# Optimization experiments

Hardware: AMD Instinct MI355X
Metric: run time of the kernel (lower is better)

Reference implementation:

```python
import jax, jax.numpy as jnp
import numpy as np

N, E = 50000, 800000
IN_DIM, OUT_DIM, REL_DIM = 128, 64, 32
NEG_SLOPE = 0.01  # torch F.leaky_relu default


def setup_inputs() -> dict:
    key = jax.random.key(0)
    ks = jax.random.split(key, 12)
    return {
        "h": jax.random.normal(ks[0], (N, IN_DIM), jnp.float32),
        "relation": jax.random.normal(ks[1], (E, REL_DIM), jnp.float32),
        "score": jax.random.normal(ks[2], (E, 1), jnp.float32),
        "timestamp": jax.random.normal(ks[3], (E, 1), jnp.float32),
        "src": jax.random.randint(ks[4], (E,), 0, N, jnp.int32),
        "dst": jax.random.randint(ks[5], (E,), 0, N, jnp.int32),
        "W_n": jax.random.normal(ks[6], (IN_DIM, OUT_DIM), jnp.float32) / np.sqrt(IN_DIM),
        "W_r": jax.random.normal(ks[7], (REL_DIM, OUT_DIM), jnp.float32) / np.sqrt(REL_DIM),
        "W_s": jax.random.normal(ks[8], (1, OUT_DIM), jnp.float32),
        "W_t": jax.random.normal(ks[9], (1, OUT_DIM), jnp.float32),
        "a": jax.random.normal(ks[10], (5 * OUT_DIM,), jnp.float32) / np.sqrt(5 * OUT_DIM),
    }


def reference(h, relation, score, timestamp, src, dst, W_n, W_r, W_s, W_t, a):
    D = W_n.shape[1]
    z = h @ W_n                     # (N, D)
    er = relation @ W_r             # (E, D)
    es = score @ W_s                # (E, D)
    et = timestamp @ W_t            # (E, D)
    z_src = z[src]                  # (E, D) gather
    z_dst = z[dst]                  # (E, D) gather
    # attn_fc on concat([z_src, z_dst, er, es, et]) == sum of slice dot-products
    a1, a2, a3, a4, a5 = (a[0:D], a[D:2*D], a[2*D:3*D], a[3*D:4*D], a[4*D:5*D])
    logit = z_src @ a1 + z_dst @ a2 + er @ a3 + es @ a4 + et @ a5  # (E,)
    logit = jnp.where(logit >= 0, logit, NEG_SLOPE * logit)        # leaky_relu
    # segment softmax over edges grouped by dst node
    n = z.shape[0]
    seg_max = jax.ops.segment_max(logit, dst, num_segments=n)     # (N,)
    ex = jnp.exp(logit - seg_max[dst])                             # (E,)
    seg_sum = jax.ops.segment_sum(ex, dst, num_segments=n)        # (N,)
    alpha = ex / seg_sum[dst]                                      # (E,)
    # weighted scatter-sum of source features to dst nodes
    h_out = jax.ops.segment_sum(alpha[:, None] * z_src, dst, num_segments=n)  # (N, D)
    return h_out
```

## Files before the change

### kernel.cpp

```cpp
#include <hip/hip_runtime.h>

#define IN_DIM 128
#define OUT_DIM 64
#define REL_DIM 32
#define NEG_SLOPE 0.01f

__global__ void k_consts(const float* __restrict__ W_r, const float* __restrict__ W_s,
                         const float* __restrict__ W_t, const float* __restrict__ a,
                         float* __restrict__ consts ) {
    int t = threadIdx.x;
    if (t < REL_DIM) {
        const float* a3 = a + 2 * OUT_DIM;
        float acc = 0.f;
        for (int d = 0; d < OUT_DIM; ++d) acc += W_r[t * OUT_DIM + d] * a3[d];
        consts[t] = acc;
    } else if (t == 32) {
        float acc = 0.f;
        for (int d = 0; d < OUT_DIM; ++d) acc += W_s[d] * a[3 * OUT_DIM + d];
        consts[32] = acc;
    } else if (t == 33) {
        float acc = 0.f;
        for (int d = 0; d < OUT_DIM; ++d) acc += W_t[d] * a[4 * OUT_DIM + d];
        consts[33] = acc;
    }
}

__global__ __launch_bounds__(256) void k_node(const float* __restrict__ h,
                                              const float* __restrict__ W_n,
                                              const float* __restrict__ a,
                                              float* __restrict__ z,
                                              float* __restrict__ s1,
                                              float* __restrict__ s2, int n) {
    __shared__ float hs[IN_DIM * 65];
    __shared__ float s1p[4][64], s2p[4][64];
    int base = blockIdx.x * 64;

    for (int i = threadIdx.x; i < 64 * 32; i += 256) {
        int r = i >> 5;
        int c4 = i & 31;
        float4 v = make_float4(0.f, 0.f, 0.f, 0.f);
        if (base + r < n) v = ((const float4*)(h + (size_t)(base + r) * IN_DIM))[c4];
        int k0 = c4 * 4;
        hs[(k0 + 0) * 65 + r] = v.x;
        hs[(k0 + 1) * 65 + r] = v.y;
        hs[(k0 + 2) * 65 + r] = v.z;
        hs[(k0 + 3) * 65 + r] = v.w;
    }
    __syncthreads();

    int lane = threadIdx.x & 63;
    int w = __builtin_amdgcn_readfirstlane(threadIdx.x >> 6);
    int c0 = w * 16;
    int row = base + lane;

    float acc[16];
    #pragma unroll
    for (int j = 0; j < 16; ++j) acc[j] = 0.f;

    const float* __restrict__ Wslice = W_n + c0;
    #pragma unroll 4
    for (int k = 0; k < IN_DIM; ++k) {
        float hv = hs[k * 65 + lane];
        const float* __restrict__ Wr = Wslice + k * OUT_DIM;
        #pragma unroll
        for (int j = 0; j < 16; ++j) acc[j] = fmaf(hv, Wr[j], acc[j]);
    }

    float p1 = 0.f, p2 = 0.f;
    #pragma unroll
    for (int j = 0; j < 16; ++j) {
        p1 = fmaf(acc[j], a[c0 + j], p1);
        p2 = fmaf(acc[j], a[OUT_DIM + c0 + j], p2);
    }
    s1p[w][lane] = p1;
    s2p[w][lane] = p2;

    if (row < n) {
        float4* zp = (float4*)(z + (size_t)row * OUT_DIM + c0);
        zp[0] = make_float4(acc[0], acc[1], acc[2], acc[3]);
        zp[1] = make_float4(acc[4], acc[5], acc[6], acc[7]);
        zp[2] = make_float4(acc[8], acc[9], acc[10], acc[11]);
        zp[3] = make_float4(acc[12], acc[13], acc[14], acc[15]);
    }
    __syncthreads();
    if (threadIdx.x < 64 && base + (int)threadIdx.x < n) {
        int l = threadIdx.x;
        s1[base + l] = s1p[0][l] + s1p[1][l] + s1p[2][l] + s1p[3][l];
        s2[base + l] = s2p[0][l] + s2p[1][l] + s2p[2][l] + s2p[3][l];
    }
}

__global__ __launch_bounds__(256) void k_count(const int* __restrict__ dst,
                                               int* __restrict__ deg, int E) {
    for (int e = blockIdx.x * blockDim.x + threadIdx.x; e < E;
         e += gridDim.x * blockDim.x)
        atomicAdd(deg + dst[e], 1);
}

__global__ __launch_bounds__(256) void k_scan1(const int* __restrict__ deg,
                                               int* __restrict__ incl,
                                               int* __restrict__ partial, int n) {
    __shared__ int tmp[256];
    int i = blockIdx.x * 256 + threadIdx.x;
    int v = (i < n) ? deg[i] : 0;
    tmp[threadIdx.x] = v;
    __syncthreads();
    #pragma unroll
    for (int o = 1; o < 256; o <<= 1) {
        int t = (threadIdx.x >= o) ? tmp[threadIdx.x - o] : 0;
        __syncthreads();
        tmp[threadIdx.x] += t;
        __syncthreads();
    }
    if (i < n) incl[i] = tmp[threadIdx.x];
    if (threadIdx.x == 255) partial[blockIdx.x] = tmp[255];
}

__global__ __launch_bounds__(256) void k_scan2(int* __restrict__ partial, int nb) {
    __shared__ int tmp[256];
    int v = (threadIdx.x < nb) ? partial[threadIdx.x] : 0;
    tmp[threadIdx.x] = v;
    __syncthreads();
    #pragma unroll
    for (int o = 1; o < 256; o <<= 1) {
        int t = (threadIdx.x >= o) ? tmp[threadIdx.x - o] : 0;
        __syncthreads();
        tmp[threadIdx.x] += t;
        __syncthreads();
    }
    if (threadIdx.x < nb) partial[threadIdx.x] = tmp[threadIdx.x] - v;
}

__global__ __launch_bounds__(256) void k_scan3(const int* __restrict__ deg,
                                               const int* __restrict__ incl,
                                               const int* __restrict__ partial,
                                               int* __restrict__ off,
                                               int* __restrict__ cnt, int n, int E) {
    int i = blockIdx.x * 256 + threadIdx.x;
    if (i < n) {
        int o = incl[i] - deg[i] + partial[i >> 8];
        off[i] = o;
        cnt[i] = o;
    }
    if (i == 0) off[n] = E;
}

__global__ __launch_bounds__(256) void k_fill(const float* __restrict__ rel,
                                              const float* __restrict__ score,
                                              const float* __restrict__ ts,
                                              const int* __restrict__ src,
                                              const int* __restrict__ dst,
                                              const float* __restrict__ s1,
                                              const float* __restrict__ s2,
                                              const float* __restrict__ consts,
                                              int* __restrict__ cnt,
                                              int2* __restrict__ pedge, int E) {
    __shared__ float wra3[REL_DIM];
    __shared__ float c45[2];
    if (threadIdx.x < REL_DIM) wra3[threadIdx.x] = consts[threadIdx.x];
    if (threadIdx.x == 32) c45[0] = consts[32];
    if (threadIdx.x == 33) c45[1] = consts[33];
    __syncthreads();
    for (int e = blockIdx.x * blockDim.x + threadIdx.x; e < E;
         e += gridDim.x * blockDim.x) {
        const float4* r4 = (const float4*)(rel + (size_t)e * REL_DIM);
        float acc = 0.f;
        #pragma unroll
        for (int j = 0; j < REL_DIM / 4; ++j) {
            float4 v = r4[j];
            acc += v.x * wra3[4 * j] + v.y * wra3[4 * j + 1] +
                   v.z * wra3[4 * j + 2] + v.w * wra3[4 * j + 3];
        }
        int s = src[e], d = dst[e];
        float lg = s1[s] + s2[d] + acc + score[e] * c45[0] + ts[e] * c45[1];
        lg = (lg >= 0.f) ? lg : NEG_SLOPE * lg;
        int pos = atomicAdd(cnt + d, 1);
        pedge[pos] = make_int2(s, __float_as_int(lg));
    }
}

__global__ __launch_bounds__(256) void k_out(const int* __restrict__ off,
                                             const int2* __restrict__ pedge,
                                             const float* __restrict__ z,
                                             float* __restrict__ out, int n) {
    int lane = threadIdx.x & 63;
    int wave = (blockIdx.x * blockDim.x + threadIdx.x) >> 6;
    int nwaves = (gridDim.x * blockDim.x) >> 6;
    int eg = lane >> 4;
    int dl = lane & 15;
    for (int node = wave; node < n; node += nwaves) {
        int start = off[node], end = off[node + 1];
        int deg = end - start;
        float4 acc = make_float4(0.f, 0.f, 0.f, 0.f);
        if (deg > 0 && deg <= 64) {
            int2 pe = make_int2(0, (int)0xff800000u);
            if (lane < deg) pe = pedge[start + lane];
            float v = __int_as_float(pe.y);
            float m = v;
            #pragma unroll
            for (int o = 32; o > 0; o >>= 1) m = fmaxf(m, __shfl_xor(m, o, 64));
            float ex = __expf(v - m);
            float ssum = ex;
            #pragma unroll
            for (int o = 32; o > 0; o >>= 1) ssum += __shfl_xor(ssum, o, 64);
            float alpha = ex * (1.0f / ssum);
            for (int j0 = 0; j0 < deg; j0 += 4) {
                int j = j0 + eg;
                int jc = (j < 64) ? j : 63;
                float wj = __shfl(alpha, jc, 64);
                int  sj = __shfl(pe.x, jc, 64);
                if (j < deg) {
                    float4 zv = ((const float4*)(z + (size_t)sj * OUT_DIM))[dl];
                    acc.x = fmaf(wj, zv.x, acc.x);
                    acc.y = fmaf(wj, zv.y, acc.y);
                    acc.z = fmaf(wj, zv.z, acc.z);
                    acc.w = fmaf(wj, zv.w, acc.w);
                }
            }
        } else if (deg > 64) {
            float m = -3.4e38f;
            for (int j = start + lane; j < end; j += 64)
                m = fmaxf(m, __int_as_float(pedge[j].y));
            #pragma unroll
            for (int o = 32; o > 0; o >>= 1) m = fmaxf(m, __shfl_xor(m, o, 64));
            float ssum = 0.f;
            for (int j = start + lane; j < end; j += 64)
                ssum += __expf(__int_as_float(pedge[j].y) - m);
            #pragma unroll
            for (int o = 32; o > 0; o >>= 1) ssum += __shfl_xor(ssum, o, 64);
            float inv = 1.0f / ssum;
            for (int j0 = start; j0 < end; j0 += 4) {
                int j = j0 + eg;
                if (j < end) {
                    int2 pe = pedge[j];
                    float wj = __expf(__int_as_float(pe.y) - m) * inv;
                    float4 zv = ((const float4*)(z + (size_t)pe.x * OUT_DIM))[dl];
                    acc.x = fmaf(wj, zv.x, acc.x);
                    acc.y = fmaf(wj, zv.y, acc.y);
                    acc.z = fmaf(wj, zv.z, acc.z);
                    acc.w = fmaf(wj, zv.w, acc.w);
                }
            }
        }
        #pragma unroll
        for (int o = 16; o <= 32; o <<= 1) {
            acc.x += __shfl_xor(acc.x, o, 64);
            acc.y += __shfl_xor(acc.y, o, 64);
            acc.z += __shfl_xor(acc.z, o, 64);
            acc.w += __shfl_xor(acc.w, o, 64);
        }
        if (eg == 0) ((float4*)(out + (size_t)node * OUT_DIM))[dl] = acc;
    }
}

extern "C" void kernel_launch(void* const* d_in, const int* in_sizes, int n_in,
                              void* d_out, int out_size, void* d_ws, size_t ws_size,
                              hipStream_t stream) {
    const float* h         = (const float*)d_in[0];
    const float* relation  = (const float*)d_in[1];
    const float* score     = (const float*)d_in[2];
    const float* timestamp = (const float*)d_in[3];
    const int*   src       = (const int*)d_in[4];
    const int*   dst       = (const int*)d_in[5];
    const float* W_n       = (const float*)d_in[6];
    const float* W_r       = (const float*)d_in[7];
    const float* W_s       = (const float*)d_in[8];
    const float* W_t       = (const float*)d_in[9];
    const float* a         = (const float*)d_in[10];

    int n = in_sizes[0] / IN_DIM;
    int E = in_sizes[4];
    int nb1 = (n + 255) / 256;

    float* ws      = (float*)d_ws;
    float* z       = ws;
    float* s1      = z + (size_t)n * OUT_DIM;
    float* s2      = s1 + n;
    float* consts  = s2 + n;
    int2*  pedge   = (int2*)(consts + 64);
    int*   deg     = (int*)(pedge + E);
    int*   incl    = deg + n;
    int*   off     = incl + n;
    int*   cnt     = off + n + 1;
    int*   partial = cnt + n;

    float* out = (float*)d_out;

    hipMemsetAsync(deg, 0, (size_t)n * sizeof(int), stream);

    k_consts<<<1, 64, 0, stream>>>(W_r, W_s, W_t, a, consts);
    k_node<<<(n + 63) / 64, 256, 0, stream>>>(h, W_n, a, z, s1, s2, n);
    k_count<<<2048, 256, 0, stream>>>(dst, deg, E);
    k_scan1<<<nb1, 256, 0, stream>>>(deg, incl, partial, n);
    k_scan2<<<1, 256, 0, stream>>>(partial, nb1);
    k_scan3<<<nb1, 256, 0, stream>>>(deg, incl, partial, off, cnt, n, E);
    k_fill<<<2048, 256, 0, stream>>>(relation, score, timestamp, src, dst,
                                     s1, s2, consts, cnt, pedge, E);
    k_out<<<(n + 3) / 4, 256, 0, stream>>>(off, pedge, z, out, n);
}
```

Baseline: 323.9 us.

## Fuse logit computation with degree count and pack edges into 32-bit words

Logit computation moves into the degree-counting pass, which now writes a per-edge 32-bit payload. The payload packs a 16-bit source index with an fp16 leaky-relu logit. The scatter pass then only moves payloads by dst, and the output kernel reads half as many bytes per edge. The constants kernel and the degree memset are folded into other kernels, and streaming inputs use nontemporal loads. The trade-offs are reduced logit precision and a packing that only holds when the node count fits in 16 bits.

```diff
diff --git a/kernel.cpp b/kernel.cpp
--- a/kernel.cpp
+++ b/kernel.cpp
@@ -1,28 +1,21 @@
 #include <hip/hip_runtime.h>
+#include <hip/hip_fp16.h>
 
 #define IN_DIM 128
 #define OUT_DIM 64
 #define REL_DIM 32
 #define NEG_SLOPE 0.01f
 
-__global__ void k_consts(const float* __restrict__ W_r, const float* __restrict__ W_s,
-                         const float* __restrict__ W_t, const float* __restrict__ a,
-                         float* __restrict__ consts ) {
-    int t = threadIdx.x;
-    if (t < REL_DIM) {
-        const float* a3 = a + 2 * OUT_DIM;
-        float acc = 0.f;
-        for (int d = 0; d < OUT_DIM; ++d) acc += W_r[t * OUT_DIM + d] * a3[d];
-        consts[t] = acc;
-    } else if (t == 32) {
-        float acc = 0.f;
-        for (int d = 0; d < OUT_DIM; ++d) acc += W_s[d] * a[3 * OUT_DIM + d];
-        consts[32] = acc;
-    } else if (t == 33) {
-        float acc = 0.f;
-        for (int d = 0; d < OUT_DIM; ++d) acc += W_t[d] * a[4 * OUT_DIM + d];
-        consts[33] = acc;
-    }
+typedef float    vfloat4 __attribute__((ext_vector_type(4)));
+typedef unsigned vuint4  __attribute__((ext_vector_type(4)));
+typedef int      vint4   __attribute__((ext_vector_type(4)));
+
+__device__ __forceinline__ unsigned pack_edge(int s, float lg) {
+    return ((unsigned)s << 16) | (unsigned)__half_as_ushort(__float2half(lg));
+}
+__device__ __forceinline__ int unpack_src(unsigned u) { return (int)(u >> 16); }
+__device__ __forceinline__ float unpack_lg(unsigned u) {
+    return __half2float(__ushort_as_half((unsigned short)(u & 0xffffu)));
 }
 
 __global__ __launch_bounds__(256) void k_node(const float* __restrict__ h,
@@ -30,7 +23,8 @@
                                               const float* __restrict__ a,
                                               float* __restrict__ z,
                                               float* __restrict__ s1,
-                                              float* __restrict__ s2, int n) {
+                                              float* __restrict__ s2,
+                                              int* __restrict__ deg, int n) {
     __shared__ float hs[IN_DIM * 65];
     __shared__ float s1p[4][64], s2p[4][64];
     int base = blockIdx.x * 64;
@@ -87,14 +81,59 @@
         int l = threadIdx.x;
         s1[base + l] = s1p[0][l] + s1p[1][l] + s1p[2][l] + s1p[3][l];
         s2[base + l] = s2p[0][l] + s2p[1][l] + s2p[2][l] + s2p[3][l];
-    }
-}
-
-__global__ __launch_bounds__(256) void k_count(const int* __restrict__ dst,
+        deg[base + l] = 0;
+    }
+}
+
+__global__ __launch_bounds__(256) void k_edge2(const float* __restrict__ rel,
+                                               const float* __restrict__ score,
+                                               const float* __restrict__ ts,
+                                               const int* __restrict__ src,
+                                               const int* __restrict__ dst,
+                                               const float* __restrict__ s1,
+                                               const float* __restrict__ s2,
+                                               const float* __restrict__ W_r,
+                                               const float* __restrict__ W_s,
+                                               const float* __restrict__ W_t,
+                                               const float* __restrict__ a,
+                                               unsigned* __restrict__ payload,
                                                int* __restrict__ deg, int E) {
+    __shared__ float wra3[REL_DIM];
+    __shared__ float c45[2];
+    int t = threadIdx.x;
+    if (t < REL_DIM) {
+        const float* a3 = a + 2 * OUT_DIM;
+        float acc = 0.f;
+        for (int d = 0; d < OUT_DIM; ++d) acc += W_r[t * OUT_DIM + d] * a3[d];
+        wra3[t] = acc;
+    } else if (t == 32 || t == 33) {
+        const float* Wx = (t == 32) ? W_s : W_t;
+        const float* ax = a + (t == 32 ? 3 : 4) * OUT_DIM;
+        float acc = 0.f;
+        for (int d = 0; d < OUT_DIM; ++d) acc += Wx[d] * ax[d];
+        c45[t - 32] = acc;
+    }
+    __syncthreads();
+    float c4 = c45[0], c5 = c45[1];
     for (int e = blockIdx.x * blockDim.x + threadIdx.x; e < E;
-         e += gridDim.x * blockDim.x)
-        atomicAdd(deg + dst[e], 1);
+         e += gridDim.x * blockDim.x) {
+        const vfloat4* r4 = (const vfloat4*)(rel + (size_t)e * REL_DIM);
+        float acc = 0.f;
+        #pragma unroll
+        for (int j = 0; j < REL_DIM / 4; ++j) {
+            vfloat4 v = __builtin_nontemporal_load(r4 + j);
+            acc += v.x * wra3[4 * j] + v.y * wra3[4 * j + 1] +
+                   v.z * wra3[4 * j + 2] + v.w * wra3[4 * j + 3];
+        }
+        int s = __builtin_nontemporal_load(src + e);
+        int d = __builtin_nontemporal_load(dst + e);
+        float sc = __builtin_nontemporal_load(score + e);
+        float tv = __builtin_nontemporal_load(ts + e);
+        float lg = s1[s] + s2[d] + acc + sc * c4 + tv * c5;
+        lg = (lg >= 0.f) ? lg : NEG_SLOPE * lg;
+        __builtin_nontemporal_store(pack_edge(s, lg), payload + e);
+        atomicAdd(deg + d, 1);
+    }
 }
 
 __global__ __launch_bounds__(256) void k_scan1(const int* __restrict__ deg,
@@ -145,42 +184,31 @@
     if (i == 0) off[n] = E;
 }
 
-__global__ __launch_bounds__(256) void k_fill(const float* __restrict__ rel,
-                                              const float* __restrict__ score,
-                                              const float* __restrict__ ts,
-                                              const int* __restrict__ src,
+__global__ __launch_bounds__(256) void k_fill(const unsigned* __restrict__ payload,
                                               const int* __restrict__ dst,
-                                              const float* __restrict__ s1,
-                                              const float* __restrict__ s2,
-                                              const float* __restrict__ consts,
                                               int* __restrict__ cnt,
-                                              int2* __restrict__ pedge, int E) {
-    __shared__ float wra3[REL_DIM];
-    __shared__ float c45[2];
-    if (threadIdx.x < REL_DIM) wra3[threadIdx.x] = consts[threadIdx.x];
-    if (threadIdx.x == 32) c45[0] = consts[32];
-    if (threadIdx.x == 33) c45[1] = consts[33];
-    __syncthreads();
-    for (int e = blockIdx.x * blockDim.x + threadIdx.x; e < E;
-         e += gridDim.x * blockDim.x) {
-        const float4* r4 = (const float4*)(rel + (size_t)e * REL_DIM);
-        float acc = 0.f;
-        #pragma unroll
-        for (int j = 0; j < REL_DIM / 4; ++j) {
-            float4 v = r4[j];
-            acc += v.x * wra3[4 * j] + v.y * wra3[4 * j + 1] +
-                   v.z * wra3[4 * j + 2] + v.w * wra3[4 * j + 3];
+                                              unsigned* __restrict__ pedge, int E) {
+    int i0 = (blockIdx.x * blockDim.x + threadIdx.x) * 4;
+    int stride = gridDim.x * blockDim.x * 4;
+    for (int i = i0; i < E; i += stride) {
+        if (i + 3 < E) {
+            vuint4 pay = __builtin_nontemporal_load((const vuint4*)(payload + i));
+            vint4  dd  = __builtin_nontemporal_load((const vint4*)(dst + i));
+            pedge[atomicAdd(cnt + dd.x, 1)] = pay.x;
+            pedge[atomicAdd(cnt + dd.y, 1)] = pay.y;
+            pedge[atomicAdd(cnt + dd.z, 1)] = pay.z;
+            pedge[atomicAdd(cnt + dd.w, 1)] = pay.w;
+        } else {
+            for (int j = i; j < E; ++j) {
+                unsigned p = payload[j];
+                pedge[atomicAdd(cnt + dst[j], 1)] = p;
+            }
         }
-        int s = src[e], d = dst[e];
-        float lg = s1[s] + s2[d] + acc + score[e] * c45[0] + ts[e] * c45[1];
-        lg = (lg >= 0.f) ? lg : NEG_SLOPE * lg;
-        int pos = atomicAdd(cnt + d, 1);
-        pedge[pos] = make_int2(s, __float_as_int(lg));
     }
 }
 
 __global__ __launch_bounds__(256) void k_out(const int* __restrict__ off,
-                                             const int2* __restrict__ pedge,
+                                             const unsigned* __restrict__ pedge,
                                              const float* __restrict__ z,
                                              float* __restrict__ out, int n) {
     int lane = threadIdx.x & 63;
@@ -193,9 +221,9 @@
         int deg = end - start;
         float4 acc = make_float4(0.f, 0.f, 0.f, 0.f);
         if (deg > 0 && deg <= 64) {
-            int2 pe = make_int2(0, (int)0xff800000u);
+            unsigned pe = 0xfc00u;
             if (lane < deg) pe = pedge[start + lane];
-            float v = __int_as_float(pe.y);
+            float v = unpack_lg(pe);
             float m = v;
             #pragma unroll
             for (int o = 32; o > 0; o >>= 1) m = fmaxf(m, __shfl_xor(m, o, 64));
@@ -204,11 +232,12 @@
             #pragma unroll
             for (int o = 32; o > 0; o >>= 1) ssum += __shfl_xor(ssum, o, 64);
             float alpha = ex * (1.0f / ssum);
+            int   srcl  = unpack_src(pe);
             for (int j0 = 0; j0 < deg; j0 += 4) {
                 int j = j0 + eg;
                 int jc = (j < 64) ? j : 63;
                 float wj = __shfl(alpha, jc, 64);
-                int  sj = __shfl(pe.x, jc, 64);
+                int  sj = __shfl(srcl, jc, 64);
                 if (j < deg) {
                     float4 zv = ((const float4*)(z + (size_t)sj * OUT_DIM))[dl];
                     acc.x = fmaf(wj, zv.x, acc.x);
@@ -220,21 +249,21 @@
         } else if (deg > 64) {
             float m = -3.4e38f;
             for (int j = start + lane; j < end; j += 64)
-                m = fmaxf(m, __int_as_float(pedge[j].y));
+                m = fmaxf(m, unpack_lg(pedge[j]));
             #pragma unroll
             for (int o = 32; o > 0; o >>= 1) m = fmaxf(m, __shfl_xor(m, o, 64));
             float ssum = 0.f;
             for (int j = start + lane; j < end; j += 64)
-                ssum += __expf(__int_as_float(pedge[j].y) - m);
+                ssum += __expf(unpack_lg(pedge[j]) - m);
             #pragma unroll
             for (int o = 32; o > 0; o >>= 1) ssum += __shfl_xor(ssum, o, 64);
             float inv = 1.0f / ssum;
             for (int j0 = start; j0 < end; j0 += 4) {
                 int j = j0 + eg;
                 if (j < end) {
-                    int2 pe = pedge[j];
-                    float wj = __expf(__int_as_float(pe.y) - m) * inv;
-                    float4 zv = ((const float4*)(z + (size_t)pe.x * OUT_DIM))[dl];
+                    unsigned pe = pedge[j];
+                    float wj = __expf(unpack_lg(pe) - m) * inv;
+                    float4 zv = ((const float4*)(z + (size_t)unpack_src(pe) * OUT_DIM))[dl];
                     acc.x = fmaf(wj, zv.x, acc.x);
                     acc.y = fmaf(wj, zv.y, acc.y);
                     acc.z = fmaf(wj, zv.z, acc.z);
@@ -272,29 +301,26 @@
     int E = in_sizes[4];
     int nb1 = (n + 255) / 256;
 
-    float* ws      = (float*)d_ws;
-    float* z       = ws;
-    float* s1      = z + (size_t)n * OUT_DIM;
-    float* s2      = s1 + n;
-    float* consts  = s2 + n;
-    int2*  pedge   = (int2*)(consts + 64);
-    int*   deg     = (int*)(pedge + E);
-    int*   incl    = deg + n;
-    int*   off     = incl + n;
-    int*   cnt     = off + n + 1;
-    int*   partial = cnt + n;
+    float*    ws      = (float*)d_ws;
+    float*    z       = ws;
+    float*    s1      = z + (size_t)n * OUT_DIM;
+    float*    s2      = s1 + n;
+    unsigned* payload = (unsigned*)(s2 + n);
+    unsigned* pedge   = payload + E;
+    int*      deg     = (int*)(pedge + E);
+    int*      incl    = deg + n;
+    int*      off     = incl + n;
+    int*      cnt     = off + n + 1;
+    int*      partial = cnt + n;
 
     float* out = (float*)d_out;
 
-    hipMemsetAsync(deg, 0, (size_t)n * sizeof(int), stream);
-
-    k_consts<<<1, 64, 0, stream>>>(W_r, W_s, W_t, a, consts);
-    k_node<<<(n + 63) / 64, 256, 0, stream>>>(h, W_n, a, z, s1, s2, n);
-    k_count<<<2048, 256, 0, stream>>>(dst, deg, E);
+    k_node<<<(n + 63) / 64, 256, 0, stream>>>(h, W_n, a, z, s1, s2, deg, n);
+    k_edge2<<<1024, 256, 0, stream>>>(relation, score, timestamp, src, dst,
+                                      s1, s2, W_r, W_s, W_t, a, payload, deg, E);
     k_scan1<<<nb1, 256, 0, stream>>>(deg, incl, partial, n);
     k_scan2<<<1, 256, 0, stream>>>(partial, nb1);
     k_scan3<<<nb1, 256, 0, stream>>>(deg, incl, partial, off, cnt, n, E);
-    k_fill<<<2048, 256, 0, stream>>>(relation, score, timestamp, src, dst,
-                                     s1, s2, consts, cnt, pedge, E);
+    k_fill<<<800, 256, 0, stream>>>(payload, dst, cnt, pedge, E);
     k_out<<<(n + 3) / 4, 256, 0, stream>>>(off, pedge, z, out, n);
 }
```

After: 342.2 us. +5.6%, slower.
